# Kernel tuning notes

Hardware: AMD Instinct MI355X
Metric: run time of the kernel (lower is better)

The kernel has to match this reference:

```python
import jax, jax.numpy as jnp
import numpy as np

T, B, D, U = 256, 128, 1024, 1024

def _orthogonal(key, shape, gain=1.0, dtype=jnp.float32):
    # Orthogonal init matching tf.initializers.Orthogonal
    n_rows, n_cols = shape
    big = max(n_rows, n_cols)
    a = jax.random.normal(key, (big, min(n_rows, n_cols)), dtype=jnp.float32)
    q, r = jnp.linalg.qr(a)
    q = q * jnp.sign(jnp.diag(r))
    q = q[:n_rows, :n_cols] if n_rows >= n_cols else q.T[:n_rows, :n_cols]
    return (gain * q).astype(dtype)

def setup_inputs() -> dict:
    key = jax.random.key(0)
    k1, k2, k3, k4 = jax.random.split(key, 4)
    inputs = jax.random.normal(k1, (T, B, D), dtype=jnp.float32)
    states = jnp.zeros((2, B, U), dtype=jnp.float32)  # stacked (c, h)
    masks = jax.random.randint(k2, (T, B), 0, 2).astype(jnp.int32)
    kernelx = _orthogonal(k3, (D, 4 * U), gain=1.0)
    kernelh = _orthogonal(k4, (U, 4 * U), gain=1.0)
    bias = jnp.zeros((4 * U,), dtype=jnp.float32)
    return {"inputs": inputs, "states": states, "masks": masks,
            "kernelx": kernelx, "kernelh": kernelh, "bias": bias}

def reference(inputs, states, masks, kernelx, kernelh, bias):
    c0, h0 = states[0], states[1]
    # mask semantics from source: m = 1 - masks; state is zeroed where mask==1
    m = (1.0 - masks.astype(inputs.dtype))[..., None]       # [T, B, 1]
    # Precompute input contribution for all steps (one big GEMM)
    xz = jnp.einsum('tbd,dk->tbk', inputs, kernelx) + bias  # [T, B, 4U]

    def step(carry, xs):
        c, h = carry
        xz_t, m_t = xs
        c = c * m_t
        h = h * m_t
        z = xz_t + h @ kernelh                              # [B, 4U]
        i, f, o, u = jnp.split(z, 4, axis=-1)
        i = jax.nn.sigmoid(i)
        f = jax.nn.sigmoid(f)
        o = jax.nn.sigmoid(o)
        u = jnp.tanh(u)
        c = f * c + i * u
        h = o * jnp.tanh(c)
        return (c, h), h

    (c, h), out = jax.lax.scan(step, (c0, h0), (xz, m))
    return out, jnp.stack([c, h])
```

## Files before the change

kernel.cpp:

```cpp
#include <hip/hip_runtime.h>


typedef float  f32x4 __attribute__((ext_vector_type(4)));
typedef float  f32x2 __attribute__((ext_vector_type(2)));
typedef __bf16 bf16x8 __attribute__((ext_vector_type(8)));
typedef unsigned short us8 __attribute__((ext_vector_type(8)));
typedef unsigned short us4 __attribute__((ext_vector_type(4)));
typedef unsigned int   u32x4 __attribute__((ext_vector_type(4)));

#define TT 256
#define BB 128
#define DD 1024
#define UU 1024
#define NZ 4096

typedef __attribute__((address_space(3))) unsigned       lds_u32;
typedef const __attribute__((address_space(1))) unsigned glob_u32;

__device__ __forceinline__ unsigned short f2bf(float x) {
  union { float f; unsigned u; } v; v.f = x;
  unsigned r = v.u + 0x7fffu + ((v.u >> 16) & 1u);
  return (unsigned short)(r >> 16);
}
__device__ __forceinline__ float bf2f(unsigned short b) {
  union { unsigned u; float f; } v; v.u = ((unsigned)b) << 16;
  return v.f;
}
__device__ __forceinline__ float sigm(float x) { return 1.f / (1.f + __expf(-x)); }
__device__ __forceinline__ float tanh_(float x) { return 1.f - 2.f / (__expf(2.f * x) + 1.f); }

__global__ __launch_bounds__(256) void k_convert(const float* __restrict__ in,
                                                 unsigned short* __restrict__ out,
                                                 int n8) {
  int i = blockIdx.x * 256 + threadIdx.x;
  if (i >= n8) return;
  const float4 a = *(const float4*)(in + (size_t)i * 8);
  const float4 b = *(const float4*)(in + (size_t)i * 8 + 4);
  us8 v;
  v[0] = f2bf(a.x); v[1] = f2bf(a.y); v[2] = f2bf(a.z); v[3] = f2bf(a.w);
  v[4] = f2bf(b.x); v[5] = f2bf(b.y); v[6] = f2bf(b.z); v[7] = f2bf(b.w);
  *(us8*)(out + (size_t)i * 8) = v;
}

__global__ __launch_bounds__(256) void k_transpose(const float* __restrict__ in,
                                                   unsigned short* __restrict__ out) {
  __shared__ unsigned short tile[64][72];
  const int ni = blockIdx.x;
  const int ki = blockIdx.y;
  const int t = threadIdx.x;
  const int c = t & 63, r0 = t >> 6;
#pragma unroll
  for (int rr = 0; rr < 16; ++rr) {
    int r = r0 * 16 + rr;
    tile[r][c] = f2bf(in[(size_t)(ki * 64 + r) * NZ + ni * 64 + c]);
  }
  __syncthreads();
  const int kcol = t & 63, ng = t >> 6;
#pragma unroll
  for (int cc = 0; cc < 16; ++cc) {
    int n_off = ng * 16 + cc;
    out[(size_t)(ni * 64 + n_off) * DD + ki * 64 + kcol] = tile[kcol][n_off];
  }
}

__global__ __launch_bounds__(256, 2) void k_gemm_bf(const unsigned short* __restrict__ A,
                                                    const unsigned short* __restrict__ Bt,
                                                    unsigned short* __restrict__ C) {
  __shared__ unsigned short Al[2][128 * 64];
  __shared__ unsigned short Bl[2][128 * 64];
  const int bx = blockIdx.x;
  const int wgid = (bx & 7) * 1024 + (bx >> 3);
  const int tm = wgid >> 5, tn = wgid & 31;
  const int tid = threadIdx.x;
  const int wave = tid >> 6, lane = tid & 63;
  const int wr = wave >> 1, wc = wave & 1;
  const int l15 = lane & 15, kg = lane >> 4;

  f32x4 acc[4][4] = {};

  const int srow = tid >> 3;
  const int scol = (tid & 7) * 8;
  const unsigned sdst = tid * 8;

  auto stage = [&](int buf, int kt) {
#pragma unroll
    for (int i = 0; i < 4; ++i) {
      __builtin_amdgcn_global_load_lds(
          (glob_u32*)(A  + (size_t)(tm * 128 + i * 32 + srow) * DD + kt * 64 + scol),
          (lds_u32*)&Al[buf][i * 2048 + sdst], 16, 0, 0);
      __builtin_amdgcn_global_load_lds(
          (glob_u32*)(Bt + (size_t)(tn * 128 + i * 32 + srow) * DD + kt * 64 + scol),
          (lds_u32*)&Bl[buf][i * 2048 + sdst], 16, 0, 0);
    }
  };

  stage(0, 0);
  __syncthreads();

  for (int kt = 0; kt < 16; ++kt) {
    const int buf = kt & 1;
    if (kt < 15) stage(buf ^ 1, kt + 1);
#pragma unroll
    for (int ks = 0; ks < 2; ++ks) {
      bf16x8 af[4], bfr[4];
#pragma unroll
      for (int mi = 0; mi < 4; ++mi)
        af[mi] = *(const bf16x8*)&Al[buf][(wr * 64 + mi * 16 + l15) * 64 + ks * 32 + kg * 8];
#pragma unroll
      for (int ni = 0; ni < 4; ++ni)
        bfr[ni] = *(const bf16x8*)&Bl[buf][(wc * 64 + ni * 16 + l15) * 64 + ks * 32 + kg * 8];
#pragma unroll
      for (int mi = 0; mi < 4; ++mi)
#pragma unroll
        for (int ni = 0; ni < 4; ++ni)
          acc[ni][mi] = __builtin_amdgcn_mfma_f32_16x16x32_bf16(bfr[ni], af[mi], acc[ni][mi], 0, 0, 0);
    }
    __syncthreads();
  }

#pragma unroll
  for (int mi = 0; mi < 4; ++mi) {
    const size_t row = (size_t)tm * 128 + wr * 64 + mi * 16 + l15;
#pragma unroll
    for (int ni = 0; ni < 4; ++ni) {
      const size_t col = (size_t)tn * 128 + wc * 64 + ni * 16 + kg * 4;
      us4 v;
      v[0] = f2bf(acc[ni][mi][0]); v[1] = f2bf(acc[ni][mi][1]);
      v[2] = f2bf(acc[ni][mi][2]); v[3] = f2bf(acc[ni][mi][3]);
      *(us4*)(C + row * NZ + col) = v;
    }
  }
}

#define SCAN_QUARTER(Q, VMSTR)                                                  \
  {                                                                             \
    asm volatile("s_waitcnt " VMSTR ::: "memory");                              \
    __builtin_amdgcn_sched_barrier(0);                                          \
    *(u32x4*)(hlds_c + sbase + (Q) * 512)         = sv[(Q) * 2];                \
    *(u32x4*)(hlds_c + sbase + 16384 + (Q) * 512) = sv[(Q) * 2 + 1];            \
    asm volatile("s_waitcnt lgkmcnt(0)" ::: "memory");                          \
    __builtin_amdgcn_sched_barrier(0);                                          \
    __builtin_amdgcn_s_barrier();                                               \
    _Pragma("unroll")                                                           \
    for (int ks = (Q) * 8; ks < (Q) * 8 + 8; ++ks) {                            \
      const char* p = ((ks & 1) ? hp1 : hp0) + (ks >> 1) * 128;                 \
      bf16x8 a = *(const bf16x8*)p;                                             \
      acc0 = __builtin_amdgcn_mfma_f32_16x16x32_bf16(a, __builtin_bit_cast(bf16x8, w0[ks]), acc0, 0, 0, 0); \
      acc1 = __builtin_amdgcn_mfma_f32_16x16x32_bf16(a, __builtin_bit_cast(bf16x8, w1[ks]), acc1, 0, 0, 0); \
    }                                                                           \
  }

__global__ __launch_bounds__(256, 1) void k_scan(const float* __restrict__ init_cs,
                                                 const int* __restrict__ masks,
                                                 const unsigned short* __restrict__ WhT,
                                                 const float* __restrict__ bias,
                                                 const unsigned short* __restrict__ xz,
                                                 float* __restrict__ out,
                                                 unsigned short* __restrict__ hglob,
                                                 unsigned* __restrict__ flags) {
  __shared__ char  hlds_c[32768];
  __shared__ float zlds[4][16][33];
  __shared__ int   mlds[TT * 16 + 16];

  const int tid = threadIdx.x;
  const int wave = tid >> 6, lane = tid & 63;
  const int l15 = lane & 15, kg = lane >> 4;
  const int blk = blockIdx.x;
  const int g = blk & 7;
  const int sb = blk >> 3;
  const int u0 = sb * 32;
  const int row0 = g * 16;
  unsigned* fl = flags + g * 64;

  u32x4 w0[32], w1[32];
  {
    const size_t r0 = (size_t)(wave * UU + u0 + l15) * DD;
    const size_t r1 = (size_t)(wave * UU + u0 + 16 + l15) * DD;
#pragma unroll
    for (int ks = 0; ks < 32; ++ks) {
      w0[ks] = *(const u32x4*)(WhT + r0 + ks * 32 + kg * 8);
      w1[ks] = *(const u32x4*)(WhT + r1 + ks * 32 + kg * 8);
    }
#pragma unroll
    for (int ks = 0; ks < 32; ++ks) {
      asm volatile("" : "+v"(w0[ks]));
      asm volatile("" : "+v"(w1[ks]));
    }
  }

  for (int i = 0; i < 16; ++i) {
    int idx = i * 256 + tid;
    mlds[idx] = masks[(size_t)(idx >> 4) * BB + row0 + (idx & 15)];
  }
  if (tid < 16) mlds[TT * 16 + tid] = 0;

  const int er = tid >> 4;
  const int ec = (tid & 15) * 2;
  const int grow = row0 + er;
  const int guu = u0 + ec;

  float bs0[4], bs1[4];
#pragma unroll
  for (int gt = 0; gt < 4; ++gt) {
    bs0[gt] = bias[gt * UU + guu];
    bs1[gt] = bias[gt * UU + guu + 1];
  }

  float cv0 = init_cs[(size_t)grow * UU + guu];
  float cv1 = init_cs[(size_t)grow * UU + guu + 1];
  float hv0 = init_cs[(size_t)BB * UU + grow * UU + guu];
  float hv1 = init_cs[(size_t)BB * UU + grow * UU + guu + 1];

  const unsigned wswz = ((unsigned)(er & 7)) << 4;
  const unsigned hoff = (unsigned)er * 2048u + ((((unsigned)guu) * 2u) ^ wswz);

  {
    int m0 = masks[grow];
    float s = m0 ? 0.f : 1.f;
    char* base = (char*)hglob + (size_t)g * 32768 + hoff;
    unsigned pv = ((unsigned)f2bf(hv1 * s) << 16) | f2bf(hv0 * s);
    *(unsigned*)base = pv;
  }
  __syncthreads();
  if (tid == 0) fl[sb] = 1;
  if (wave == 0) {
    unsigned v;
    do { v = __hip_atomic_load(&fl[lane & 31], __ATOMIC_RELAXED, __HIP_MEMORY_SCOPE_AGENT); }
    while (!__all(v >= 1));
  }
  __syncthreads();

  const unsigned rswz = ((unsigned)(l15 & 7)) << 4;
  const char* hp0 = hlds_c + l15 * 2048 + (((unsigned)(kg * 16 + 0)) ^ rswz);
  const char* hp1 = hlds_c + l15 * 2048 + (((unsigned)(kg * 16 + 64)) ^ rswz);

  const unsigned sbase = ((unsigned)(tid >> 5)) * 2048u + ((unsigned)(tid & 31)) * 16u;

  for (int t = 0; t < TT; ++t) {
    const char* gsrc = (const char*)hglob + ((size_t)((t & 1) * 8 + g)) * 32768;

    u32x4 sv[8];
#pragma unroll
    for (int q = 0; q < 4; ++q) {
#pragma unroll
      for (int j = 0; j < 2; ++j) {
        const char* ap = gsrc + sbase + j * 16384 + q * 512;
        asm volatile("global_load_dwordx4 %0, %1, off sc0" : "=v"(sv[q * 2 + j]) : "v"(ap));
      }
    }

    f32x4 acc0 = {0.f, 0.f, 0.f, 0.f};
    f32x4 acc1 = {0.f, 0.f, 0.f, 0.f};

    SCAN_QUARTER(0, "vmcnt(6)")
    SCAN_QUARTER(1, "vmcnt(4)")

    unsigned xzv[4];
    {
      const size_t xrow = ((size_t)(t * BB + grow)) * NZ;
#pragma unroll
      for (int gt = 0; gt < 4; ++gt)
        xzv[gt] = *(const unsigned*)(xz + xrow + gt * UU + guu);
    }

    SCAN_QUARTER(2, "vmcnt(6)")
    SCAN_QUARTER(3, "vmcnt(4)")

#pragma unroll
    for (int j = 0; j < 4; ++j) {
      zlds[wave][kg * 4 + j][l15] = acc0[j];
      zlds[wave][kg * 4 + j][16 + l15] = acc1[j];
    }
    __syncthreads();

    const int mcur = mlds[t * 16 + er];
    const int mnxt = mlds[(t + 1) * 16 + er];
    float z0[4], z1[4];
#pragma unroll
    for (int gt = 0; gt < 4; ++gt) {
      z0[gt] = zlds[gt][er][ec]     + bs0[gt] + bf2f((unsigned short)(xzv[gt] & 0xffffu));
      z1[gt] = zlds[gt][er][ec + 1] + bs1[gt] + bf2f((unsigned short)(xzv[gt] >> 16));
    }
    const float sm = mcur ? 0.f : 1.f;
    cv0 *= sm; cv1 *= sm;
    {
      float ig = sigm(z0[0]), fg = sigm(z0[1]), og = sigm(z0[2]), ug = tanh_(z0[3]);
      cv0 = fg * cv0 + ig * ug;
      hv0 = og * tanh_(cv0);
    }
    {
      float ig = sigm(z1[0]), fg = sigm(z1[1]), og = sigm(z1[2]), ug = tanh_(z1[3]);
      cv1 = fg * cv1 + ig * ug;
      hv1 = og * tanh_(cv1);
    }

    {
      const float sn = mnxt ? 0.f : 1.f;
      char* hdst = (char*)hglob + ((size_t)(((t + 1) & 1) * 8 + g)) * 32768 + hoff;
      unsigned pv = ((unsigned)f2bf(hv1 * sn) << 16) | f2bf(hv0 * sn);
      asm volatile("global_store_dword %0, %1, off" :: "v"(hdst), "v"(pv) : "memory");
      float* odst = out + (size_t)t * (BB * UU) + (size_t)grow * UU + guu;
      f32x2 ov = {hv0, hv1};
      asm volatile("global_store_dwordx2 %0, %1, off" :: "v"(odst), "v"(ov) : "memory");
    }
    asm volatile("s_waitcnt vmcnt(1)" ::: "memory");
    __builtin_amdgcn_sched_barrier(0);
    __builtin_amdgcn_s_barrier();
    if (tid == 0) fl[sb] = (unsigned)(t + 2);
    if (wave == 0) {
      const unsigned tgt = (unsigned)(t + 2);
      unsigned v;
      do { v = __hip_atomic_load(&fl[lane & 31], __ATOMIC_RELAXED, __HIP_MEMORY_SCOPE_AGENT); }
      while (!__all(v >= tgt));
    }
    __builtin_amdgcn_s_barrier();
  }

  float* so = out + (size_t)TT * BB * UU;
  *(f32x2*)(so + (size_t)grow * UU + guu) = (f32x2){cv0, cv1};
  *(f32x2*)(so + (size_t)BB * UU + grow * UU + guu) = (f32x2){hv0, hv1};
}

extern "C" void kernel_launch(void* const* d_in, const int* in_sizes, int n_in,
                              void* d_out, int out_size, void* d_ws, size_t ws_size,
                              hipStream_t stream) {
  const float* inputs  = (const float*)d_in[0];
  const float* states  = (const float*)d_in[1];
  const int*   masks   = (const int*)d_in[2];
  const float* kernelx = (const float*)d_in[3];
  const float* kernelh = (const float*)d_in[4];
  const float* bias    = (const float*)d_in[5];
  float* out = (float*)d_out;
  char* ws = (char*)d_ws;

  unsigned* flags       = (unsigned*)ws;
  unsigned short* hglob = (unsigned short*)(ws + 65536);
  unsigned short* WhT   = (unsigned short*)(ws + (size_t)2  * 1048576);
  unsigned short* WxT   = (unsigned short*)(ws + (size_t)10 * 1048576);
  unsigned short* Abf   = (unsigned short*)(ws + (size_t)18 * 1048576);
  unsigned short* xzbig = (unsigned short*)(ws + (size_t)82 * 1048576);

  k_transpose<<<dim3(64, 16), dim3(256), 0, stream>>>(kernelx, WxT);
  k_transpose<<<dim3(64, 16), dim3(256), 0, stream>>>(kernelh, WhT);
  k_convert<<<dim3(16384), dim3(256), 0, stream>>>(inputs, Abf, (TT * BB * DD) / 8);
  k_gemm_bf<<<dim3(8192), dim3(256), 0, stream>>>(Abf, WxT, xzbig);
  hipMemsetAsync(flags, 0, 2048, stream);
  k_scan<<<dim3(256), dim3(256), 0, stream>>>(states, masks, WhT, bias, xzbig,
                                              out, hglob, flags);
}
```

Baseline: 1.199 ms.

## Prefetch next-step xz and let every wave poll the cross-block flags

The xz gate input for step t+1 is now loaded at the top of step t, so its latency overlaps the h-load and MFMA phase instead of sitting in the middle of it. The vmcnt waits are adjusted for the extra loads in flight. Every wave now spins on the global step flags itself, which drops the trailing workgroup barrier after the poll. The cost is more atomic polling traffic and a few extra registers for the double-buffered xz values.

```diff
diff --git a/kernel.cpp b/kernel.cpp
--- a/kernel.cpp
+++ b/kernel.cpp
@@ -223,18 +223,25 @@
   }
   __syncthreads();
   if (tid == 0) fl[sb] = 1;
-  if (wave == 0) {
+  {
     unsigned v;
     do { v = __hip_atomic_load(&fl[lane & 31], __ATOMIC_RELAXED, __HIP_MEMORY_SCOPE_AGENT); }
     while (!__all(v >= 1));
   }
-  __syncthreads();
 
   const unsigned rswz = ((unsigned)(l15 & 7)) << 4;
   const char* hp0 = hlds_c + l15 * 2048 + (((unsigned)(kg * 16 + 0)) ^ rswz);
   const char* hp1 = hlds_c + l15 * 2048 + (((unsigned)(kg * 16 + 64)) ^ rswz);
 
   const unsigned sbase = ((unsigned)(tid >> 5)) * 2048u + ((unsigned)(tid & 31)) * 16u;
+
+  unsigned xz_cur[4], xz_nxt[4];
+  {
+    const size_t xr0 = ((size_t)grow) * NZ + guu;
+#pragma unroll
+    for (int gt = 0; gt < 4; ++gt)
+      xz_cur[gt] = *(const unsigned*)(xz + xr0 + gt * UU);
+  }
 
   for (int t = 0; t < TT; ++t) {
     const char* gsrc = (const char*)hglob + ((size_t)((t & 1) * 8 + g)) * 32768;
@@ -248,38 +255,41 @@
         asm volatile("global_load_dwordx4 %0, %1, off sc0" : "=v"(sv[q * 2 + j]) : "v"(ap));
       }
     }
+    {
+      const int t1 = (t + 1 < TT) ? t + 1 : t;
+      const char* xb = (const char*)xz + (((size_t)(t1 * BB + grow)) * NZ + guu) * 2;
+#pragma unroll
+      for (int gt = 0; gt < 4; ++gt) {
+        const void* ap = xb + gt * (UU * 2);
+        asm volatile("global_load_dword %0, %1, off" : "=v"(xz_nxt[gt]) : "v"(ap));
+      }
+    }
 
     f32x4 acc0 = {0.f, 0.f, 0.f, 0.f};
     f32x4 acc1 = {0.f, 0.f, 0.f, 0.f};
 
-    SCAN_QUARTER(0, "vmcnt(6)")
-    SCAN_QUARTER(1, "vmcnt(4)")
-
-    unsigned xzv[4];
-    {
-      const size_t xrow = ((size_t)(t * BB + grow)) * NZ;
-#pragma unroll
-      for (int gt = 0; gt < 4; ++gt)
-        xzv[gt] = *(const unsigned*)(xz + xrow + gt * UU + guu);
-    }
-
-    SCAN_QUARTER(2, "vmcnt(6)")
-    SCAN_QUARTER(3, "vmcnt(4)")
+    SCAN_QUARTER(0, "vmcnt(9)")
+    SCAN_QUARTER(1, "vmcnt(7)")
+    SCAN_QUARTER(2, "vmcnt(5)")
+    SCAN_QUARTER(3, "vmcnt(3)")
 
 #pragma unroll
     for (int j = 0; j < 4; ++j) {
       zlds[wave][kg * 4 + j][l15] = acc0[j];
       zlds[wave][kg * 4 + j][16 + l15] = acc1[j];
     }
-    __syncthreads();
+    asm volatile("s_waitcnt lgkmcnt(0)" ::: "memory");
+    __builtin_amdgcn_sched_barrier(0);
+    __builtin_amdgcn_s_barrier();
+    __builtin_amdgcn_sched_barrier(0);
 
     const int mcur = mlds[t * 16 + er];
     const int mnxt = mlds[(t + 1) * 16 + er];
     float z0[4], z1[4];
 #pragma unroll
     for (int gt = 0; gt < 4; ++gt) {
-      z0[gt] = zlds[gt][er][ec]     + bs0[gt] + bf2f((unsigned short)(xzv[gt] & 0xffffu));
-      z1[gt] = zlds[gt][er][ec + 1] + bs1[gt] + bf2f((unsigned short)(xzv[gt] >> 16));
+      z0[gt] = zlds[gt][er][ec]     + bs0[gt] + bf2f((unsigned short)(xz_cur[gt] & 0xffffu));
+      z1[gt] = zlds[gt][er][ec + 1] + bs1[gt] + bf2f((unsigned short)(xz_cur[gt] >> 16));
     }
     const float sm = mcur ? 0.f : 1.f;
     cv0 *= sm; cv1 *= sm;
@@ -307,13 +317,15 @@
     __builtin_amdgcn_sched_barrier(0);
     __builtin_amdgcn_s_barrier();
     if (tid == 0) fl[sb] = (unsigned)(t + 2);
-    if (wave == 0) {
+    {
       const unsigned tgt = (unsigned)(t + 2);
       unsigned v;
       do { v = __hip_atomic_load(&fl[lane & 31], __ATOMIC_RELAXED, __HIP_MEMORY_SCOPE_AGENT); }
       while (!__all(v >= tgt));
     }
-    __builtin_amdgcn_s_barrier();
+
+#pragma unroll
+    for (int gt = 0; gt < 4; ++gt) xz_cur[gt] = xz_nxt[gt];
   }
 
   float* so = out + (size_t)TT * BB * UU;
```

New measurement: 1.233 ms. 2.8% more time.
